# Kernel tuning notes

Hardware: AMD Instinct MI355X
Metric: run time of the kernel (lower is better)

## Reference

```python
import jax, jax.numpy as jnp
import numpy as np

BN_EPS = 1e-5
LN_EPS = 1e-5


def setup_inputs() -> dict:
    key = jax.random.key(0)
    ks = jax.random.split(key, 8)
    B, D, T = 16, 96, 512  # batch, enc_in (channels), d_model (time/feature)
    H = 2 * T
    residual = jax.random.normal(ks[0], (B, D, T), dtype=jnp.float32)
    # BatchNorm1d(enc_in) affine params
    bn_gamma = jnp.ones((D,), dtype=jnp.float32)
    bn_beta = jnp.zeros((D,), dtype=jnp.float32)
    # LayerNorm(d_model) affine params
    ln_gamma = jnp.ones((T,), dtype=jnp.float32)
    ln_beta = jnp.zeros((T,), dtype=jnp.float32)
    # MLP: Linear(T, 2T) -> GELU -> Linear(2T, T)
    W1 = jax.random.normal(ks[1], (T, H), dtype=jnp.float32) / np.float32(np.sqrt(T))
    b1 = jnp.zeros((H,), dtype=jnp.float32)
    W2 = jax.random.normal(ks[2], (H, T), dtype=jnp.float32) / np.float32(np.sqrt(H))
    b2 = jnp.zeros((T,), dtype=jnp.float32)
    return {"residual": residual, "bn_gamma": bn_gamma, "bn_beta": bn_beta,
            "ln_gamma": ln_gamma, "ln_beta": ln_beta,
            "W1": W1, "b1": b1, "W2": W2, "b2": b2}


def _var_cor_attention(x):
    # x: [B, D, T]; queries = keys = values = x
    B, D, T = x.shape
    f = jnp.fft.rfft(x, axis=-1)                       # [B, D, F]
    # pairwise spectral product q_i * conj(k_j): [B, D, D, F]
    res = f[:, :, None, :] * jnp.conj(f[:, None, :, :])
    corr = jnp.fft.irfft(res, axis=-1).mean(axis=-1)   # [B, D, D]
    scale = np.float32(1.0 / np.sqrt(T))
    corr = jax.nn.softmax(corr * scale, axis=-1)
    V = jnp.einsum('bsd,bde->bse', corr, x)            # [B, D, T]
    return V


def reference(residual, bn_gamma, bn_beta, ln_gamma, ln_beta, W1, b1, W2, b2):
    # attention + residual
    x = _var_cor_attention(residual) + residual        # [B, D, T]
    # BatchNorm1d over channel dim D: stats over (B, T), biased variance
    mu = x.mean(axis=(0, 2), keepdims=True)
    var = ((x - mu) ** 2).mean(axis=(0, 2), keepdims=True)
    x = (x - mu) * jax.lax.rsqrt(var + BN_EPS)
    x = x * bn_gamma[None, :, None] + bn_beta[None, :, None]
    # MLP (exact GELU, torch default) + residual
    h = jax.nn.gelu(jnp.einsum('bdt,th->bdh', x, W1) + b1, approximate=False)
    y = jnp.einsum('bdh,ht->bdt', h, W2) + b2 + x
    # LayerNorm over last dim T
    mu2 = y.mean(axis=-1, keepdims=True)
    var2 = ((y - mu2) ** 2).mean(axis=-1, keepdims=True)
    y = (y - mu2) * jax.lax.rsqrt(var2 + LN_EPS)
    return y * ln_gamma + ln_beta
```

## Files before the change

### kernel.cpp

```cpp
#include <hip/hip_runtime.h>
#include <math.h>
#include <stdint.h>

#define BB 16
#define DD 96
#define TT 512
#define HH 1024
#define NROW (BB*DD)

typedef __attribute__((ext_vector_type(4))) float floatx4;
typedef __attribute__((ext_vector_type(8))) short short8;

#define WSOFF_X     0
#define WSOFF_HFRAG 0
#define WSOFF_XROW  (3*1024*1024)
#define WSOFF_XFRAG (WSOFF_XROW + NROW*TT*2)
#define WSOFF_W1BF  (WSOFF_XFRAG + NROW*TT*2)
#define WSOFF_W2BF  (WSOFF_W1BF + TT*HH*2)
#define WSOFF_A     (WSOFF_W2BF + HH*TT*2)
#define WSOFF_S     (WSOFF_A + BB*DD*DD*4)
#define WSOFF_SC    (WSOFF_S + NROW*4)
#define WSOFF_SH    (WSOFF_SC + DD*4)

__device__ __forceinline__ uint16_t f2bf(float v) {
    uint32_t u = __float_as_uint(v);
    uint32_t r = 0x7fffu + ((u >> 16) & 1u);
    return (uint16_t)((u + r) >> 16);
}
__device__ __forceinline__ float bf2f(uint16_t v) {
    return __uint_as_float(((uint32_t)v) << 16);
}

#define KT1 (TT/32)
#define KT2 (HH/32)
__device__ __forceinline__ size_t afrag1_slot(int row, int k) {
    return ((size_t)((row >> 4)*KT1 + (k >> 5))*64 + ((k >> 3) & 3)*16 + (row & 15));
}

__global__ __launch_bounds__(64) void k_rowsum(const float* __restrict__ r,
                                               float* __restrict__ s) {
    int row = blockIdx.x;
    int lane = threadIdx.x;
    const float* p = r + (size_t)row * TT;
    float acc = 0.f;
    #pragma unroll
    for (int i = 0; i < TT/64; ++i) acc += p[lane + i*64];
    #pragma unroll
    for (int o = 32; o > 0; o >>= 1) acc += __shfl_down(acc, o, 64);
    if (lane == 0) s[row] = acc;
}

__global__ __launch_bounds__(128) void k_softA(const float* __restrict__ s,
                                               float* __restrict__ A) {
    int b = blockIdx.x;
    int i = threadIdx.x;
    __shared__ float sl[DD];
    if (i < DD) sl[i] = s[b*DD + i];
    __syncthreads();
    if (i >= DD) return;
    const float c = 1.0f / (512.0f * 22.627416997969522f);
    float si = sl[i] * c;
    float m = -1e30f;
    for (int j = 0; j < DD; ++j) m = fmaxf(m, si * sl[j]);
    float sum = 0.f;
    for (int j = 0; j < DD; ++j) sum += expf(si * sl[j] - m);
    float inv = 1.0f / sum;
    float* Ao = A + ((size_t)b*DD + i)*DD;
    for (int j = 0; j < DD; ++j) Ao[j] = expf(si * sl[j] - m) * inv;
}

__global__ __launch_bounds__(256) void k_attn3(const float* __restrict__ r,
                                               const float* __restrict__ A,
                                               float* __restrict__ x) {
    __shared__ float rlds[DD*64];
    int b = blockIdx.x, chunk = blockIdx.y, ig = blockIdx.z;
    int tid = threadIdx.x;
    int t0 = chunk * 64;
    const float4* rb4 = reinterpret_cast<const float4*>(r + (size_t)b*DD*TT);
    float4* rl4 = reinterpret_cast<float4*>(rlds);
    #pragma unroll
    for (int s = 0; s < 6; ++s) {
        int idx = tid + s*256;
        int i = idx >> 4, t4 = idx & 15;
        rl4[idx] = rb4[(size_t)i*(TT/4) + (t0 >> 2) + t4];
    }
    __syncthreads();

    int wave = __builtin_amdgcn_readfirstlane(tid >> 6);
    int lane = tid & 63;
    int i0 = ig*24 + wave*6;
    const float* Ab = A + ((size_t)b*DD + i0)*DD;

    float acc[6];
    #pragma unroll
    for (int rr = 0; rr < 6; ++rr) acc[rr] = rlds[(i0+rr)*64 + lane];
    #pragma unroll 4
    for (int j4 = 0; j4 < DD/4; ++j4) {
        float4 a[6];
        #pragma unroll
        for (int rr = 0; rr < 6; ++rr)
            a[rr] = *reinterpret_cast<const float4*>(Ab + rr*DD + j4*4);
        float rv[4];
        #pragma unroll
        for (int u = 0; u < 4; ++u) rv[u] = rlds[(j4*4+u)*64 + lane];
        #pragma unroll
        for (int rr = 0; rr < 6; ++rr) {
            acc[rr] = fmaf(a[rr].x, rv[0], acc[rr]);
            acc[rr] = fmaf(a[rr].y, rv[1], acc[rr]);
            acc[rr] = fmaf(a[rr].z, rv[2], acc[rr]);
            acc[rr] = fmaf(a[rr].w, rv[3], acc[rr]);
        }
    }
    #pragma unroll
    for (int rr = 0; rr < 6; ++rr)
        x[((size_t)b*DD + i0 + rr)*TT + t0 + lane] = acc[rr];
}

__global__ __launch_bounds__(256) void k_bnstat(const float* __restrict__ x,
                                                const float* __restrict__ g,
                                                const float* __restrict__ bt,
                                                float* __restrict__ sc,
                                                float* __restrict__ sh) {
    int d = blockIdx.x;
    int tid = threadIdx.x;
    int half = tid >> 7;
    int t4 = tid & 127;
    float ls = 0.f, ls2 = 0.f;
    #pragma unroll
    for (int bb = 0; bb < 8; ++bb) {
        int b = bb*2 + half;
        float4 v = *reinterpret_cast<const float4*>(&x[((size_t)b*DD + d)*TT + t4*4]);
        ls  += v.x+v.y+v.z+v.w;
        ls2 += v.x*v.x+v.y*v.y+v.z*v.z+v.w*v.w;
    }
    #pragma unroll
    for (int o = 32; o > 0; o >>= 1) {
        ls  += __shfl_down(ls,  o, 64);
        ls2 += __shfl_down(ls2, o, 64);
    }
    __shared__ float r1[4], r2[4];
    int wid = tid >> 6;
    if ((tid & 63) == 0) { r1[wid] = ls; r2[wid] = ls2; }
    __syncthreads();
    if (tid == 0) {
        float s1 = r1[0]+r1[1]+r1[2]+r1[3];
        float s2 = r2[0]+r2[1]+r2[2]+r2[3];
        const float invn = 1.0f / (float)(BB*TT);
        float mu  = s1 * invn;
        float var = s2 * invn - mu*mu;
        float rs  = rsqrtf(var + 1e-5f);
        float scale = rs * g[d];
        sc[d] = scale;
        sh[d] = bt[d] - mu * scale;
    }
}

__global__ __launch_bounds__(256) void k_bnx(const float* __restrict__ x,
                                             const float* __restrict__ sc,
                                             const float* __restrict__ sh,
                                             uint16_t* __restrict__ xrow,
                                             uint16_t* __restrict__ xfrag) {
    int g = blockIdx.x*256 + threadIdx.x;
    int row = g >> 7;
    int k0 = (g & 127) * 4;
    int d = row % DD;
    float4 v = *reinterpret_cast<const float4*>(&x[(size_t)row*TT + k0]);
    float scd = sc[d], shd = sh[d];
    ushort4 o;
    o.x = f2bf(v.x*scd + shd);
    o.y = f2bf(v.y*scd + shd);
    o.z = f2bf(v.z*scd + shd);
    o.w = f2bf(v.w*scd + shd);
    *reinterpret_cast<ushort4*>(&xrow[(size_t)row*TT + k0]) = o;
    size_t slot = afrag1_slot(row, k0);
    *reinterpret_cast<ushort4*>(&xfrag[slot*8 + (k0 & 7)]) = o;
}

__global__ __launch_bounds__(64) void k_wswiz(const float* __restrict__ W1,
                                              const float* __restrict__ W2,
                                              uint16_t* __restrict__ w1bf,
                                              uint16_t* __restrict__ w2bf) {
    int blk = blockIdx.x;
    int lane = threadIdx.x;
    int q = lane >> 4, l15 = lane & 15;
    const float* W; uint16_t* out; int KT, N, b;
    if (blk < 1024) { W = W1; out = w1bf; KT = 16; N = 1024; b = blk; }
    else            { W = W2; out = w2bf; KT = 32; N = 512;  b = blk - 1024; }
    int tile_n = b / KT, tile_k = b % KT;
    const float* src = W + (size_t)(tile_k*32 + q*8)*N + tile_n*16 + l15;
    uint16_t tmp[8];
    #pragma unroll
    for (int j = 0; j < 8; ++j) tmp[j] = f2bf(src[(size_t)j*N]);
    uint16_t* dst = out + ((size_t)b*64 + lane)*8;
    *reinterpret_cast<ushort4*>(dst)     = *reinterpret_cast<ushort4*>(&tmp[0]);
    *reinterpret_cast<ushort4*>(dst + 4) = *reinterpret_cast<ushort4*>(&tmp[4]);
}

__global__ __launch_bounds__(256) void k_gemm1(const uint16_t* __restrict__ xfrag,
                                               const uint16_t* __restrict__ w1bf,
                                               const float* __restrict__ b1,
                                               uint16_t* __restrict__ hfrag) {
    __shared__ __align__(16) uint16_t cs[16][136];
    int tid = threadIdx.x;
    int wave = tid >> 6, lane = tid & 63;
    int q = lane >> 4, l15 = lane & 15;
    int mtile = blockIdx.x;
    int n0 = blockIdx.y * 128 + wave * 32;
    floatx4 acc[2] = {};
    const uint16_t* ap  = xfrag + ((size_t)mtile*KT1*64 + lane)*8;
    const uint16_t* b0p = w1bf + ((size_t)((n0>>4)    )*16*64 + lane)*8;
    const uint16_t* b1p = w1bf + ((size_t)((n0>>4) + 1)*16*64 + lane)*8;
    #pragma unroll
    for (int kk = 0; kk < 16; ++kk) {
        short8 a  = *reinterpret_cast<const short8*>(ap  + kk*512);
        short8 b0 = *reinterpret_cast<const short8*>(b0p + kk*512);
        short8 b1 = *reinterpret_cast<const short8*>(b1p + kk*512);
        acc[0] = __builtin_amdgcn_mfma_f32_16x16x32_bf16(a, b0, acc[0], 0, 0, 0);
        acc[1] = __builtin_amdgcn_mfma_f32_16x16x32_bf16(a, b1, acc[1], 0, 0, 0);
    }
    #pragma unroll
    for (int nf = 0; nf < 2; ++nf) {
        int coll = wave*32 + nf*16 + l15;
        float bias = b1[blockIdx.y*128 + coll];
        #pragma unroll
        for (int r = 0; r < 4; ++r) {
            float v = acc[nf][r] + bias;
            float gl = 0.5f * v * (1.0f + erff(v * 0.7071067811865475f));
            cs[q*4 + r][coll] = f2bf(gl);
        }
    }
    __syncthreads();
    int c = wave;
    const uint4* src = reinterpret_cast<const uint4*>(&cs[l15][c*32 + q*8]);
    size_t chunk = (size_t)mtile*KT2 + (blockIdx.y*4 + c);
    reinterpret_cast<uint4*>(hfrag)[chunk*64 + lane] = *src;
}

__global__ __launch_bounds__(256) void k_gemm2(const uint16_t* __restrict__ hfrag,
                                               const uint16_t* __restrict__ w2bf,
                                               const float* __restrict__ b2,
                                               const uint16_t* __restrict__ xrow,
                                               float* __restrict__ y) {
    int tid = threadIdx.x;
    int wave = tid >> 6, lane = tid & 63;
    int q = lane >> 4, l15 = lane & 15;
    int mtile = blockIdx.x;
    int m0 = mtile * 16;
    int n0 = blockIdx.y * 128 + wave * 32;
    floatx4 acc[2] = {};
    const uint16_t* ap  = hfrag + ((size_t)mtile*KT2*64 + lane)*8;
    const uint16_t* b0p = w2bf + ((size_t)((n0>>4)    )*32*64 + lane)*8;
    const uint16_t* b1p = w2bf + ((size_t)((n0>>4) + 1)*32*64 + lane)*8;
    #pragma unroll
    for (int kk = 0; kk < 32; ++kk) {
        short8 a  = *reinterpret_cast<const short8*>(ap  + kk*512);
        short8 b0 = *reinterpret_cast<const short8*>(b0p + kk*512);
        short8 b1 = *reinterpret_cast<const short8*>(b1p + kk*512);
        acc[0] = __builtin_amdgcn_mfma_f32_16x16x32_bf16(a, b0, acc[0], 0, 0, 0);
        acc[1] = __builtin_amdgcn_mfma_f32_16x16x32_bf16(a, b1, acc[1], 0, 0, 0);
    }
    #pragma unroll
    for (int nf = 0; nf < 2; ++nf) {
        int col = n0 + nf*16 + l15;
        float bias = b2[col];
        #pragma unroll
        for (int r = 0; r < 4; ++r) {
            int row = m0 + q*4 + r;
            float xb = bf2f(xrow[(size_t)row*TT + col]);
            y[(size_t)row*TT + col] = acc[nf][r] + bias + xb;
        }
    }
}

__global__ __launch_bounds__(64) void k_ln(float* __restrict__ y,
                                           const float* __restrict__ lng,
                                           const float* __restrict__ lnb) {
    int row = blockIdx.x;
    int lane = threadIdx.x;
    float4* p = reinterpret_cast<float4*>(y + (size_t)row*TT);
    float4 v0 = p[lane*2], v1 = p[lane*2 + 1];
    float s  = v0.x+v0.y+v0.z+v0.w + v1.x+v1.y+v1.z+v1.w;
    float s2 = v0.x*v0.x+v0.y*v0.y+v0.z*v0.z+v0.w*v0.w
             + v1.x*v1.x+v1.y*v1.y+v1.z*v1.z+v1.w*v1.w;
    #pragma unroll
    for (int o = 1; o < 64; o <<= 1) {
        s  += __shfl_xor(s,  o, 64);
        s2 += __shfl_xor(s2, o, 64);
    }
    float mu = s * (1.0f/TT);
    float var = s2 * (1.0f/TT) - mu*mu;
    float rs = rsqrtf(var + 1e-5f);
    const float4* g4 = reinterpret_cast<const float4*>(lng);
    const float4* b4 = reinterpret_cast<const float4*>(lnb);
    float4 g0 = g4[lane*2], g1 = g4[lane*2+1];
    float4 bb0 = b4[lane*2], bb1 = b4[lane*2+1];
    float4 o0, o1;
    o0.x = (v0.x-mu)*rs*g0.x + bb0.x;  o0.y = (v0.y-mu)*rs*g0.y + bb0.y;
    o0.z = (v0.z-mu)*rs*g0.z + bb0.z;  o0.w = (v0.w-mu)*rs*g0.w + bb0.w;
    o1.x = (v1.x-mu)*rs*g1.x + bb1.x;  o1.y = (v1.y-mu)*rs*g1.y + bb1.y;
    o1.z = (v1.z-mu)*rs*g1.z + bb1.z;  o1.w = (v1.w-mu)*rs*g1.w + bb1.w;
    p[lane*2] = o0;  p[lane*2+1] = o1;
}

extern "C" void kernel_launch(void* const* d_in, const int* in_sizes, int n_in,
                              void* d_out, int out_size, void* d_ws, size_t ws_size,
                              hipStream_t stream) {
    (void)in_sizes; (void)n_in; (void)out_size; (void)ws_size;
    const float* residual = (const float*)d_in[0];
    const float* bng = (const float*)d_in[1];
    const float* bnb = (const float*)d_in[2];
    const float* lng = (const float*)d_in[3];
    const float* lnb = (const float*)d_in[4];
    const float* W1  = (const float*)d_in[5];
    const float* b1  = (const float*)d_in[6];
    const float* W2  = (const float*)d_in[7];
    const float* b2  = (const float*)d_in[8];
    float* out = (float*)d_out;
    char* ws = (char*)d_ws;
    float*    x     = (float*)(ws + WSOFF_X);
    uint16_t* hfrag = (uint16_t*)(ws + WSOFF_HFRAG);
    uint16_t* xrow  = (uint16_t*)(ws + WSOFF_XROW);
    uint16_t* xfrag = (uint16_t*)(ws + WSOFF_XFRAG);
    uint16_t* w1bf  = (uint16_t*)(ws + WSOFF_W1BF);
    uint16_t* w2bf  = (uint16_t*)(ws + WSOFF_W2BF);
    float*    A     = (float*)(ws + WSOFF_A);
    float*    s     = (float*)(ws + WSOFF_S);
    float*    sc    = (float*)(ws + WSOFF_SC);
    float*    sh    = (float*)(ws + WSOFF_SH);

    k_rowsum<<<NROW, 64, 0, stream>>>(residual, s);
    k_softA<<<BB, 128, 0, stream>>>(s, A);
    k_wswiz<<<2048, 64, 0, stream>>>(W1, W2, w1bf, w2bf);
    k_attn3<<<dim3(BB, 8, 4), 256, 0, stream>>>(residual, A, x);
    k_bnstat<<<DD, 256, 0, stream>>>(x, bng, bnb, sc, sh);
    k_bnx<<<NROW*TT/1024, 256, 0, stream>>>(x, sc, sh, xrow, xfrag);
    k_gemm1<<<dim3(96, 8), 256, 0, stream>>>(xfrag, w1bf, b1, hfrag);
    k_gemm2<<<dim3(96, 4), 256, 0, stream>>>(hfrag, w2bf, b2, xrow, out);
    k_ln<<<NROW, 64, 0, stream>>>(out, lng, lnb);
}
```

Measured before the change: 122.8 us.

## Fuse pipeline into four kernels: prep, attention+weight swizzle, BN apply, fused MLP+LayerNorm

The nine-kernel pipeline becomes four. Row sums and softmax merge into one kernel. The weight bf16 swizzle shares a launch with the attention matmul, which also writes per-chunk BatchNorm partial sums, so the separate stats pass over x goes away. GEMM1+GELU, GEMM2, the residual add and LayerNorm run in one kernel that keeps the hidden activations in LDS instead of global memory. The cost is only 96 blocks for the MLP kernel, each loading all of W1 and W2 through 8 waves, which may limit parallelism and memory throughput.

```diff
diff --git a/kernel.cpp b/kernel.cpp
--- a/kernel.cpp
+++ b/kernel.cpp
@@ -12,15 +12,13 @@
 typedef __attribute__((ext_vector_type(8))) short short8;
 
 #define WSOFF_X     0
-#define WSOFF_HFRAG 0
 #define WSOFF_XROW  (3*1024*1024)
 #define WSOFF_XFRAG (WSOFF_XROW + NROW*TT*2)
 #define WSOFF_W1BF  (WSOFF_XFRAG + NROW*TT*2)
 #define WSOFF_W2BF  (WSOFF_W1BF + TT*HH*2)
 #define WSOFF_A     (WSOFF_W2BF + HH*TT*2)
-#define WSOFF_S     (WSOFF_A + BB*DD*DD*4)
-#define WSOFF_SC    (WSOFF_S + NROW*4)
-#define WSOFF_SH    (WSOFF_SC + DD*4)
+#define WSOFF_P1    (WSOFF_A + BB*DD*DD*4)
+#define WSOFF_P2    (WSOFF_P1 + DD*128*4)
 
 __device__ __forceinline__ uint16_t f2bf(float v) {
     uint32_t u = __float_as_uint(v);
@@ -32,65 +30,84 @@
 }
 
 #define KT1 (TT/32)
-#define KT2 (HH/32)
 __device__ __forceinline__ size_t afrag1_slot(int row, int k) {
     return ((size_t)((row >> 4)*KT1 + (k >> 5))*64 + ((k >> 3) & 3)*16 + (row & 15));
 }
 
-__global__ __launch_bounds__(64) void k_rowsum(const float* __restrict__ r,
-                                               float* __restrict__ s) {
-    int row = blockIdx.x;
-    int lane = threadIdx.x;
-    const float* p = r + (size_t)row * TT;
-    float acc = 0.f;
-    #pragma unroll
-    for (int i = 0; i < TT/64; ++i) acc += p[lane + i*64];
-    #pragma unroll
-    for (int o = 32; o > 0; o >>= 1) acc += __shfl_down(acc, o, 64);
-    if (lane == 0) s[row] = acc;
-}
-
-__global__ __launch_bounds__(128) void k_softA(const float* __restrict__ s,
-                                               float* __restrict__ A) {
+__global__ __launch_bounds__(256) void k_prep(const float* __restrict__ r,
+                                              float* __restrict__ A) {
+    __shared__ float sl[DD];
     int b = blockIdx.x;
-    int i = threadIdx.x;
-    __shared__ float sl[DD];
-    if (i < DD) sl[i] = s[b*DD + i];
-    __syncthreads();
-    if (i >= DD) return;
-    const float c = 1.0f / (512.0f * 22.627416997969522f);
-    float si = sl[i] * c;
-    float m = -1e30f;
-    for (int j = 0; j < DD; ++j) m = fmaxf(m, si * sl[j]);
-    float sum = 0.f;
-    for (int j = 0; j < DD; ++j) sum += expf(si * sl[j] - m);
-    float inv = 1.0f / sum;
-    float* Ao = A + ((size_t)b*DD + i)*DD;
-    for (int j = 0; j < DD; ++j) Ao[j] = expf(si * sl[j] - m) * inv;
-}
-
-__global__ __launch_bounds__(256) void k_attn3(const float* __restrict__ r,
-                                               const float* __restrict__ A,
-                                               float* __restrict__ x) {
+    int tid = threadIdx.x;
+    int w = tid >> 6, lane = tid & 63;
+    for (int rr = 0; rr < 24; ++rr) {
+        int i = w*24 + rr;
+        const float* p = r + ((size_t)b*DD + i)*TT;
+        float acc = 0.f;
+        #pragma unroll
+        for (int s = 0; s < TT/64; ++s) acc += p[lane + s*64];
+        #pragma unroll
+        for (int o = 32; o > 0; o >>= 1) acc += __shfl_down(acc, o, 64);
+        if (lane == 0) sl[i] = acc;
+    }
+    __syncthreads();
+    int i = tid;
+    if (i < DD) {
+        const float c = 1.0f / (512.0f * 22.627416997969522f);
+        float si = sl[i] * c;
+        float m = -1e30f;
+        for (int j = 0; j < DD; ++j) m = fmaxf(m, si * sl[j]);
+        float sum = 0.f;
+        for (int j = 0; j < DD; ++j) sum += expf(si * sl[j] - m);
+        float inv = 1.0f / sum;
+        float* Ao = A + ((size_t)b*DD + i)*DD;
+        for (int j = 0; j < DD; ++j) Ao[j] = expf(si * sl[j] - m) * inv;
+    }
+}
+
+__global__ __launch_bounds__(256) void k_attw(const float* __restrict__ r,
+                                              const float* __restrict__ A,
+                                              const float* __restrict__ W1,
+                                              const float* __restrict__ W2,
+                                              float* __restrict__ x,
+                                              uint16_t* __restrict__ w1bf,
+                                              uint16_t* __restrict__ w2bf,
+                                              float* __restrict__ P1,
+                                              float* __restrict__ P2) {
+    int bx = blockIdx.x;
+    int tid = threadIdx.x;
+    int w = tid >> 6, lane = tid & 63;
+    if (bx < 512) {
+        int blk = bx*4 + w;
+        int q = lane >> 4, l15 = lane & 15;
+        const float* W; uint16_t* out; int KT, N, b;
+        if (blk < 1024) { W = W1; out = w1bf; KT = 16; N = 1024; b = blk; }
+        else            { W = W2; out = w2bf; KT = 32; N = 512;  b = blk - 1024; }
+        int tile_n = b / KT, tile_k = b % KT;
+        const float* src = W + (size_t)(tile_k*32 + q*8)*N + tile_n*16 + l15;
+        uint16_t tmp[8];
+        #pragma unroll
+        for (int j = 0; j < 8; ++j) tmp[j] = f2bf(src[(size_t)j*N]);
+        uint16_t* dst = out + ((size_t)b*64 + lane)*8;
+        *reinterpret_cast<ushort4*>(dst)     = *reinterpret_cast<ushort4*>(&tmp[0]);
+        *reinterpret_cast<ushort4*>(dst + 4) = *reinterpret_cast<ushort4*>(&tmp[4]);
+        return;
+    }
     __shared__ float rlds[DD*64];
-    int b = blockIdx.x, chunk = blockIdx.y, ig = blockIdx.z;
-    int tid = threadIdx.x;
+    int idx = bx - 512;
+    int b = idx & 15, chunk = (idx >> 4) & 7, ig = idx >> 7;
     int t0 = chunk * 64;
     const float4* rb4 = reinterpret_cast<const float4*>(r + (size_t)b*DD*TT);
     float4* rl4 = reinterpret_cast<float4*>(rlds);
     #pragma unroll
     for (int s = 0; s < 6; ++s) {
-        int idx = tid + s*256;
-        int i = idx >> 4, t4 = idx & 15;
-        rl4[idx] = rb4[(size_t)i*(TT/4) + (t0 >> 2) + t4];
-    }
-    __syncthreads();
-
-    int wave = __builtin_amdgcn_readfirstlane(tid >> 6);
-    int lane = tid & 63;
-    int i0 = ig*24 + wave*6;
+        int ii = tid + s*256;
+        rl4[ii] = rb4[(size_t)(ii >> 4)*(TT/4) + (t0 >> 2) + (ii & 15)];
+    }
+    __syncthreads();
+    int wu = __builtin_amdgcn_readfirstlane(w);
+    int i0 = ig*24 + wu*6;
     const float* Ab = A + ((size_t)b*DD + i0)*DD;
-
     float acc[6];
     #pragma unroll
     for (int rr = 0; rr < 6; ++rr) acc[rr] = rlds[(i0+rr)*64 + lane];
@@ -111,61 +128,62 @@
             acc[rr] = fmaf(a[rr].w, rv[3], acc[rr]);
         }
     }
-    #pragma unroll
-    for (int rr = 0; rr < 6; ++rr)
-        x[((size_t)b*DD + i0 + rr)*TT + t0 + lane] = acc[rr];
-}
-
-__global__ __launch_bounds__(256) void k_bnstat(const float* __restrict__ x,
-                                                const float* __restrict__ g,
-                                                const float* __restrict__ bt,
-                                                float* __restrict__ sc,
-                                                float* __restrict__ sh) {
-    int d = blockIdx.x;
+    int p = b*8 + chunk;
+    #pragma unroll
+    for (int rr = 0; rr < 6; ++rr) {
+        int i = i0 + rr;
+        x[((size_t)b*DD + i)*TT + t0 + lane] = acc[rr];
+        float ls = acc[rr], ls2 = acc[rr]*acc[rr];
+        #pragma unroll
+        for (int o = 32; o > 0; o >>= 1) {
+            ls  += __shfl_down(ls,  o, 64);
+            ls2 += __shfl_down(ls2, o, 64);
+        }
+        if (lane == 0) { P1[i*128 + p] = ls; P2[i*128 + p] = ls2; }
+    }
+}
+
+__global__ __launch_bounds__(256) void k_bnx(const float* __restrict__ x,
+                                             const float* __restrict__ P1,
+                                             const float* __restrict__ P2,
+                                             const float* __restrict__ g,
+                                             const float* __restrict__ bt,
+                                             uint16_t* __restrict__ xrow,
+                                             uint16_t* __restrict__ xfrag) {
+    __shared__ float rr1[4], rr2[4], scsh[4];
+    int blk = blockIdx.x;
     int tid = threadIdx.x;
-    int half = tid >> 7;
-    int t4 = tid & 127;
-    float ls = 0.f, ls2 = 0.f;
-    #pragma unroll
-    for (int bb = 0; bb < 8; ++bb) {
-        int b = bb*2 + half;
-        float4 v = *reinterpret_cast<const float4*>(&x[((size_t)b*DD + d)*TT + t4*4]);
-        ls  += v.x+v.y+v.z+v.w;
-        ls2 += v.x*v.x+v.y*v.y+v.z*v.z+v.w*v.w;
-    }
+    int wid = tid >> 6, lane = tid & 63;
+    int r0 = blk*2;
+    int d0 = r0 % DD, d1 = (r0+1) % DD;
+    int d = (wid < 2) ? d0 : d1;
+    int p = (wid & 1)*64 + lane;
+    float v1 = P1[d*128 + p], v2 = P2[d*128 + p];
     #pragma unroll
     for (int o = 32; o > 0; o >>= 1) {
-        ls  += __shfl_down(ls,  o, 64);
-        ls2 += __shfl_down(ls2, o, 64);
-    }
-    __shared__ float r1[4], r2[4];
-    int wid = tid >> 6;
-    if ((tid & 63) == 0) { r1[wid] = ls; r2[wid] = ls2; }
-    __syncthreads();
-    if (tid == 0) {
-        float s1 = r1[0]+r1[1]+r1[2]+r1[3];
-        float s2 = r2[0]+r2[1]+r2[2]+r2[3];
+        v1 += __shfl_down(v1, o, 64);
+        v2 += __shfl_down(v2, o, 64);
+    }
+    if (lane == 0) { rr1[wid] = v1; rr2[wid] = v2; }
+    __syncthreads();
+    if (tid < 2) {
+        float s1 = rr1[tid*2] + rr1[tid*2+1];
+        float s2 = rr2[tid*2] + rr2[tid*2+1];
         const float invn = 1.0f / (float)(BB*TT);
         float mu  = s1 * invn;
         float var = s2 * invn - mu*mu;
         float rs  = rsqrtf(var + 1e-5f);
-        float scale = rs * g[d];
-        sc[d] = scale;
-        sh[d] = bt[d] - mu * scale;
-    }
-}
-
-__global__ __launch_bounds__(256) void k_bnx(const float* __restrict__ x,
-                                             const float* __restrict__ sc,
-                                             const float* __restrict__ sh,
-                                             uint16_t* __restrict__ xrow,
-                                             uint16_t* __restrict__ xfrag) {
-    int g = blockIdx.x*256 + threadIdx.x;
-    int row = g >> 7;
-    int k0 = (g & 127) * 4;
-    int d = row % DD;
+        int dd = (tid == 0) ? d0 : d1;
+        float scale = rs * g[dd];
+        scsh[tid*2]   = scale;
+        scsh[tid*2+1] = bt[dd] - mu*scale;
+    }
+    __syncthreads();
+    int half = tid >> 7;
+    int row = r0 + half;
+    int k0 = (tid & 127) * 4;
+    float scd = scsh[half*2], shd = scsh[half*2+1];
     float4 v = *reinterpret_cast<const float4*>(&x[(size_t)row*TT + k0]);
-    float scd = sc[d], shd = sh[d];
     ushort4 o;
     o.x = f2bf(v.x*scd + shd);
     o.y = f2bf(v.y*scd + shd);
@@ -176,130 +194,119 @@
     *reinterpret_cast<ushort4*>(&xfrag[slot*8 + (k0 & 7)]) = o;
 }
 
-__global__ __launch_bounds__(64) void k_wswiz(const float* __restrict__ W1,
-                                              const float* __restrict__ W2,
-                                              uint16_t* __restrict__ w1bf,
-                                              uint16_t* __restrict__ w2bf) {
-    int blk = blockIdx.x;
-    int lane = threadIdx.x;
+__global__ __launch_bounds__(512) void k_mlp(const uint16_t* __restrict__ xfrag,
+                                             const uint16_t* __restrict__ w1bf,
+                                             const uint16_t* __restrict__ w2bf,
+                                             const float* __restrict__ b1,
+                                             const float* __restrict__ b2,
+                                             const uint16_t* __restrict__ xrow,
+                                             const float* __restrict__ lng,
+                                             const float* __restrict__ lnb,
+                                             float* __restrict__ out) {
+    __shared__ __align__(16) uint16_t hls[32*512];
+    __shared__ float lnp1[16][8], lnp2[16][8];
+    __shared__ float lnmu[16], lnrs[16];
+    int tid = threadIdx.x;
+    int w = tid >> 6, lane = tid & 63;
     int q = lane >> 4, l15 = lane & 15;
-    const float* W; uint16_t* out; int KT, N, b;
-    if (blk < 1024) { W = W1; out = w1bf; KT = 16; N = 1024; b = blk; }
-    else            { W = W2; out = w2bf; KT = 32; N = 512;  b = blk - 1024; }
-    int tile_n = b / KT, tile_k = b % KT;
-    const float* src = W + (size_t)(tile_k*32 + q*8)*N + tile_n*16 + l15;
-    uint16_t tmp[8];
-    #pragma unroll
-    for (int j = 0; j < 8; ++j) tmp[j] = f2bf(src[(size_t)j*N]);
-    uint16_t* dst = out + ((size_t)b*64 + lane)*8;
-    *reinterpret_cast<ushort4*>(dst)     = *reinterpret_cast<ushort4*>(&tmp[0]);
-    *reinterpret_cast<ushort4*>(dst + 4) = *reinterpret_cast<ushort4*>(&tmp[4]);
-}
-
-__global__ __launch_bounds__(256) void k_gemm1(const uint16_t* __restrict__ xfrag,
-                                               const uint16_t* __restrict__ w1bf,
-                                               const float* __restrict__ b1,
-                                               uint16_t* __restrict__ hfrag) {
-    __shared__ __align__(16) uint16_t cs[16][136];
-    int tid = threadIdx.x;
-    int wave = tid >> 6, lane = tid & 63;
-    int q = lane >> 4, l15 = lane & 15;
-    int mtile = blockIdx.x;
-    int n0 = blockIdx.y * 128 + wave * 32;
-    floatx4 acc[2] = {};
-    const uint16_t* ap  = xfrag + ((size_t)mtile*KT1*64 + lane)*8;
-    const uint16_t* b0p = w1bf + ((size_t)((n0>>4)    )*16*64 + lane)*8;
-    const uint16_t* b1p = w1bf + ((size_t)((n0>>4) + 1)*16*64 + lane)*8;
-    #pragma unroll
-    for (int kk = 0; kk < 16; ++kk) {
-        short8 a  = *reinterpret_cast<const short8*>(ap  + kk*512);
-        short8 b0 = *reinterpret_cast<const short8*>(b0p + kk*512);
-        short8 b1 = *reinterpret_cast<const short8*>(b1p + kk*512);
-        acc[0] = __builtin_amdgcn_mfma_f32_16x16x32_bf16(a, b0, acc[0], 0, 0, 0);
-        acc[1] = __builtin_amdgcn_mfma_f32_16x16x32_bf16(a, b1, acc[1], 0, 0, 0);
-    }
-    #pragma unroll
-    for (int nf = 0; nf < 2; ++nf) {
-        int coll = wave*32 + nf*16 + l15;
-        float bias = b1[blockIdx.y*128 + coll];
+    int mtile = blockIdx.x, m0 = mtile*16;
+
+    short8 a1[16];
+    {
+        const uint16_t* ap = xfrag + ((size_t)mtile*KT1*64 + lane)*8;
+        #pragma unroll
+        for (int kk = 0; kk < KT1; ++kk)
+            a1[kk] = *reinterpret_cast<const short8*>(ap + kk*512);
+    }
+    #pragma unroll
+    for (int nf = 0; nf < 8; ++nf) {
+        floatx4 acc = {};
+        const uint16_t* bp = w1bf + (((size_t)(w*8 + nf))*16*64 + lane)*8;
+        #pragma unroll
+        for (int kk = 0; kk < 16; ++kk) {
+            short8 b = *reinterpret_cast<const short8*>(bp + kk*512);
+            acc = __builtin_amdgcn_mfma_f32_16x16x32_bf16(a1[kk], b, acc, 0, 0, 0);
+        }
+        int hcol = w*128 + nf*16 + l15;
+        float bias = b1[hcol];
+        int base = (hcol >> 5)*512 + (((hcol >> 3) & 3)*16)*8 + (hcol & 7);
         #pragma unroll
         for (int r = 0; r < 4; ++r) {
-            float v = acc[nf][r] + bias;
+            float v = acc[r] + bias;
             float gl = 0.5f * v * (1.0f + erff(v * 0.7071067811865475f));
-            cs[q*4 + r][coll] = f2bf(gl);
-        }
-    }
-    __syncthreads();
-    int c = wave;
-    const uint4* src = reinterpret_cast<const uint4*>(&cs[l15][c*32 + q*8]);
-    size_t chunk = (size_t)mtile*KT2 + (blockIdx.y*4 + c);
-    reinterpret_cast<uint4*>(hfrag)[chunk*64 + lane] = *src;
-}
-
-__global__ __launch_bounds__(256) void k_gemm2(const uint16_t* __restrict__ hfrag,
-                                               const uint16_t* __restrict__ w2bf,
-                                               const float* __restrict__ b2,
-                                               const uint16_t* __restrict__ xrow,
-                                               float* __restrict__ y) {
-    int tid = threadIdx.x;
-    int wave = tid >> 6, lane = tid & 63;
-    int q = lane >> 4, l15 = lane & 15;
-    int mtile = blockIdx.x;
-    int m0 = mtile * 16;
-    int n0 = blockIdx.y * 128 + wave * 32;
-    floatx4 acc[2] = {};
-    const uint16_t* ap  = hfrag + ((size_t)mtile*KT2*64 + lane)*8;
-    const uint16_t* b0p = w2bf + ((size_t)((n0>>4)    )*32*64 + lane)*8;
-    const uint16_t* b1p = w2bf + ((size_t)((n0>>4) + 1)*32*64 + lane)*8;
-    #pragma unroll
-    for (int kk = 0; kk < 32; ++kk) {
-        short8 a  = *reinterpret_cast<const short8*>(ap  + kk*512);
-        short8 b0 = *reinterpret_cast<const short8*>(b0p + kk*512);
-        short8 b1 = *reinterpret_cast<const short8*>(b1p + kk*512);
-        acc[0] = __builtin_amdgcn_mfma_f32_16x16x32_bf16(a, b0, acc[0], 0, 0, 0);
-        acc[1] = __builtin_amdgcn_mfma_f32_16x16x32_bf16(a, b1, acc[1], 0, 0, 0);
-    }
-    #pragma unroll
-    for (int nf = 0; nf < 2; ++nf) {
-        int col = n0 + nf*16 + l15;
+            int row = q*4 + r;
+            hls[base + row*8] = f2bf(gl);
+        }
+    }
+    __syncthreads();
+
+    floatx4 acc2[4] = {};
+    for (int half = 0; half < 2; ++half) {
+        short8 a2[16];
+        #pragma unroll
+        for (int kk = 0; kk < 16; ++kk)
+            a2[kk] = *reinterpret_cast<const short8*>(&hls[(half*16 + kk)*512 + lane*8]);
+        #pragma unroll
+        for (int nf2 = 0; nf2 < 4; ++nf2) {
+            const uint16_t* bp = w2bf + (((size_t)(w*4 + nf2)*32 + half*16)*64 + lane)*8;
+            #pragma unroll
+            for (int kk = 0; kk < 16; ++kk) {
+                short8 b = *reinterpret_cast<const short8*>(bp + kk*512);
+                acc2[nf2] = __builtin_amdgcn_mfma_f32_16x16x32_bf16(a2[kk], b, acc2[nf2], 0, 0, 0);
+            }
+        }
+    }
+    float ya[4][4];
+    float p1[4] = {0,0,0,0}, p2[4] = {0,0,0,0};
+    #pragma unroll
+    for (int nf2 = 0; nf2 < 4; ++nf2) {
+        int col = w*64 + nf2*16 + l15;
         float bias = b2[col];
         #pragma unroll
         for (int r = 0; r < 4; ++r) {
-            int row = m0 + q*4 + r;
-            float xb = bf2f(xrow[(size_t)row*TT + col]);
-            y[(size_t)row*TT + col] = acc[nf][r] + bias + xb;
-        }
-    }
-}
-
-__global__ __launch_bounds__(64) void k_ln(float* __restrict__ y,
-                                           const float* __restrict__ lng,
-                                           const float* __restrict__ lnb) {
-    int row = blockIdx.x;
-    int lane = threadIdx.x;
-    float4* p = reinterpret_cast<float4*>(y + (size_t)row*TT);
-    float4 v0 = p[lane*2], v1 = p[lane*2 + 1];
-    float s  = v0.x+v0.y+v0.z+v0.w + v1.x+v1.y+v1.z+v1.w;
-    float s2 = v0.x*v0.x+v0.y*v0.y+v0.z*v0.z+v0.w*v0.w
-             + v1.x*v1.x+v1.y*v1.y+v1.z*v1.z+v1.w*v1.w;
-    #pragma unroll
-    for (int o = 1; o < 64; o <<= 1) {
-        s  += __shfl_xor(s,  o, 64);
-        s2 += __shfl_xor(s2, o, 64);
-    }
-    float mu = s * (1.0f/TT);
-    float var = s2 * (1.0f/TT) - mu*mu;
-    float rs = rsqrtf(var + 1e-5f);
-    const float4* g4 = reinterpret_cast<const float4*>(lng);
-    const float4* b4 = reinterpret_cast<const float4*>(lnb);
-    float4 g0 = g4[lane*2], g1 = g4[lane*2+1];
-    float4 bb0 = b4[lane*2], bb1 = b4[lane*2+1];
-    float4 o0, o1;
-    o0.x = (v0.x-mu)*rs*g0.x + bb0.x;  o0.y = (v0.y-mu)*rs*g0.y + bb0.y;
-    o0.z = (v0.z-mu)*rs*g0.z + bb0.z;  o0.w = (v0.w-mu)*rs*g0.w + bb0.w;
-    o1.x = (v1.x-mu)*rs*g1.x + bb1.x;  o1.y = (v1.y-mu)*rs*g1.y + bb1.y;
-    o1.z = (v1.z-mu)*rs*g1.z + bb1.z;  o1.w = (v1.w-mu)*rs*g1.w + bb1.w;
-    p[lane*2] = o0;  p[lane*2+1] = o1;
+            int row = q*4 + r;
+            float v = acc2[nf2][r] + bias + bf2f(xrow[(size_t)(m0+row)*TT + col]);
+            ya[nf2][r] = v;
+            p1[r] += v;
+            p2[r] += v*v;
+        }
+    }
+    #pragma unroll
+    for (int r = 0; r < 4; ++r) {
+        #pragma unroll
+        for (int o = 1; o < 16; o <<= 1) {
+            p1[r] += __shfl_xor(p1[r], o, 64);
+            p2[r] += __shfl_xor(p2[r], o, 64);
+        }
+    }
+    if (l15 == 0) {
+        #pragma unroll
+        for (int r = 0; r < 4; ++r) {
+            lnp1[q*4 + r][w] = p1[r];
+            lnp2[q*4 + r][w] = p2[r];
+        }
+    }
+    __syncthreads();
+    if (tid < 16) {
+        float s1 = 0.f, s2 = 0.f;
+        #pragma unroll
+        for (int ww = 0; ww < 8; ++ww) { s1 += lnp1[tid][ww]; s2 += lnp2[tid][ww]; }
+        float mu = s1 * (1.0f/TT);
+        float var = s2 * (1.0f/TT) - mu*mu;
+        lnmu[tid] = mu;
+        lnrs[tid] = rsqrtf(var + 1e-5f);
+    }
+    __syncthreads();
+    #pragma unroll
+    for (int nf2 = 0; nf2 < 4; ++nf2) {
+        int col = w*64 + nf2*16 + l15;
+        float gg = lng[col], bb = lnb[col];
+        #pragma unroll
+        for (int r = 0; r < 4; ++r) {
+            int row = q*4 + r;
+            out[(size_t)(m0+row)*TT + col] = (ya[nf2][r] - lnmu[row]) * lnrs[row] * gg + bb;
+        }
+    }
 }
 
 extern "C" void kernel_launch(void* const* d_in, const int* in_sizes, int n_in,
@@ -318,23 +325,16 @@
     float* out = (float*)d_out;
     char* ws = (char*)d_ws;
     float*    x     = (float*)(ws + WSOFF_X);
-    uint16_t* hfrag = (uint16_t*)(ws + WSOFF_HFRAG);
     uint16_t* xrow  = (uint16_t*)(ws + WSOFF_XROW);
     uint16_t* xfrag = (uint16_t*)(ws + WSOFF_XFRAG);
     uint16_t* w1bf  = (uint16_t*)(ws + WSOFF_W1BF);
     uint16_t* w2bf  = (uint16_t*)(ws + WSOFF_W2BF);
     float*    A     = (float*)(ws + WSOFF_A);
-    float*    s     = (float*)(ws + WSOFF_S);
-    float*    sc    = (float*)(ws + WSOFF_SC);
-    float*    sh    = (float*)(ws + WSOFF_SH);
-
-    k_rowsum<<<NROW, 64, 0, stream>>>(residual, s);
-    k_softA<<<BB, 128, 0, stream>>>(s, A);
-    k_wswiz<<<2048, 64, 0, stream>>>(W1, W2, w1bf, w2bf);
-    k_attn3<<<dim3(BB, 8, 4), 256, 0, stream>>>(residual, A, x);
-    k_bnstat<<<DD, 256, 0, stream>>>(x, bng, bnb, sc, sh);
-    k_bnx<<<NROW*TT/1024, 256, 0, stream>>>(x, sc, sh, xrow, xfrag);
-    k_gemm1<<<dim3(96, 8), 256, 0, stream>>>(xfrag, w1bf, b1, hfrag);
-    k_gemm2<<<dim3(96, 4), 256, 0, stream>>>(hfrag, w2bf, b2, xrow, out);
-    k_ln<<<NROW, 64, 0, stream>>>(out, lng, lnb);
-}
+    float*    P1    = (float*)(ws + WSOFF_P1);
+    float*    P2    = (float*)(ws + WSOFF_P2);
+
+    k_prep<<<BB, 256, 0, stream>>>(residual, A);
+    k_attw<<<1024, 256, 0, stream>>>(residual, A, W1, W2, x, w1bf, w2bf, P1, P2);
+    k_bnx<<<NROW/2, 256, 0, stream>>>(x, P1, P2, bng, bnb, xrow, xfrag);
+    k_mlp<<<DD, 512, 0, stream>>>(xfrag, w1bf, w2bf, b1, b2, xrow, lng, lnb, out);
+}
```

Result: slower. 157.5 us (+28.3%).
